# Kernel tuning notes

Hardware: AMD Instinct MI355X
Metric: run time of the kernel (lower is better)

The kernel has to match this reference:

```python
import jax, jax.numpy as jnp
import numpy as np

TEMPERATURE = 0.2
EPS = 1e-12

def _l2norm(x):
    # F.normalize(dim=1): x / max(||x||, eps)
    n = jnp.sqrt(jnp.sum(x * x, axis=1, keepdims=True))
    return x / jnp.maximum(n, EPS)

def setup_inputs() -> dict:
    key = jax.random.key(0)
    k1, k2, k3 = jax.random.split(key, 3)
    B, D, Q = 1024, 128, 65536
    return {
        "global_features_1": jax.random.normal(k1, (B, D), dtype=jnp.float32),
        "global_features_2": jax.random.normal(k2, (B, D), dtype=jnp.float32),
        "queue": jax.random.normal(k3, (Q, D), dtype=jnp.float32),
    }

def reference(global_features_1, global_features_2, queue):
    q = _l2norm(global_features_1)                    # [B, D]
    k = _l2norm(global_features_2)                    # [B, D]
    pos_sim = jnp.sum(q * k, axis=1, keepdims=True) / TEMPERATURE   # [B, 1]
    # queue renormalized under no_grad in the original
    queue_n = jax.lax.stop_gradient(_l2norm(queue))   # [Q, D]
    neg_sim = jnp.einsum('bd,qd->bq', q, queue_n) / TEMPERATURE     # [B, Q]
    logits = jnp.concatenate([pos_sim, neg_sim], axis=1)            # [B, 1+Q]
    # cross-entropy with label 0 for every row: -log_softmax(logits)[:, 0]
    log_probs = jax.nn.log_softmax(logits, axis=1)
    loss = -jnp.mean(log_probs[:, 0])
    return (loss, pos_sim, neg_sim)
```

## Files before the change

### kernel.cpp

```cpp
#include <hip/hip_runtime.h>
#include <math.h>

constexpr int B = 1024;
constexpr int D = 128;
constexpr int Q = 65536;
constexpr int NPART = 1024;
#define TEMP_INV 5.0f
#define EPS 1e-12f

typedef __bf16 bf16x8 __attribute__((ext_vector_type(8)));
typedef float  f32x4  __attribute__((ext_vector_type(4)));

__device__ __forceinline__ float wave_reduce_sum(float v) {
    #pragma unroll
    for (int off = 32; off > 0; off >>= 1) v += __shfl_xor(v, off);
    return v;
}

__device__ __forceinline__ unsigned short f2bf(float x) {
    unsigned int u = __float_as_uint(x);
    unsigned int r = (u + 0x7FFFu + ((u >> 16) & 1u)) >> 16;
    return (unsigned short)r;
}

__global__ __launch_bounds__(256) void k_prep(const float* __restrict__ g1,
                                              const float* __restrict__ g2,
                                              const float* __restrict__ queue,
                                              unsigned short* __restrict__ qnb,
                                              unsigned short* __restrict__ qb,
                                              float* __restrict__ out_pos,
                                              float* __restrict__ ws_pos) {
    if (blockIdx.x < Q / 8) {
        int half = threadIdx.x >> 5;
        int l    = threadIdx.x & 31;
        int row  = blockIdx.x * 8 + half;
        const f32x4* src = (const f32x4*)(queue + (size_t)row * D);
        f32x4 v = __builtin_nontemporal_load(&src[l]);
        float ss = v.x * v.x + v.y * v.y + v.z * v.z + v.w * v.w;
        #pragma unroll
        for (int off = 16; off > 0; off >>= 1) ss += __shfl_xor(ss, off);
        float inv = 1.0f / fmaxf(sqrtf(ss), EPS);
        uint2 o;
        o.x = (unsigned int)f2bf(v.x * inv) | ((unsigned int)f2bf(v.y * inv) << 16);
        o.y = (unsigned int)f2bf(v.z * inv) | ((unsigned int)f2bf(v.w * inv) << 16);
        ((uint2*)(qb + (size_t)row * D))[l] = o;
    } else {
        int idx = blockIdx.x - Q / 8;
        int w2 = threadIdx.x >> 7;
        int tt = threadIdx.x & 127;
        int b  = idx * 2 + w2;
        int w  = tt >> 6, lane = tt & 63;
        float x = g1[b * D + tt];
        float y = g2[b * D + tt];
        __shared__ float sx[2][2], sy[2][2], sp[2][2];
        float xs = wave_reduce_sum(x * x);
        float ys = wave_reduce_sum(y * y);
        if (lane == 0) { sx[w2][w] = xs; sy[w2][w] = ys; }
        __syncthreads();
        float ix = 1.0f / fmaxf(sqrtf(sx[w2][0] + sx[w2][1]), EPS);
        float iy = 1.0f / fmaxf(sqrtf(sy[w2][0] + sy[w2][1]), EPS);
        float qv = x * ix;
        float kv = y * iy;
        qnb[b * D + tt] = f2bf(qv);
        float p = wave_reduce_sum(qv * kv);
        if (lane == 0) sp[w2][w] = p;
        __syncthreads();
        if (tt == 0) {
            float pos = (sp[w2][0] + sp[w2][1]) * TEMP_INV;
            out_pos[b] = pos;
            ws_pos[b]  = pos;
        }
    }
}

__global__ __launch_bounds__(256, 3) void k_gemm_mfma(const unsigned short* __restrict__ qnb,
                                                      const unsigned short* __restrict__ qb,
                                                      float* __restrict__ neg,
                                                      float* __restrict__ psum) {
    __shared__ unsigned short As[128][72];
    __shared__ unsigned short Bs[128][72];
    const int t  = threadIdx.x;
    const int blk = blockIdx.x;
    const int bx = blk >> 3;
    const int by = blk & 7;
    const int R0 = by * 128, C0 = bx * 128;
    const int wid = t >> 6, lane = t & 63;
    const int wr = wid >> 1, wc = wid & 1;
    const int lg = lane >> 4, lc = lane & 15;

    f32x4 acc[4][4];
    #pragma unroll
    for (int m = 0; m < 4; ++m)
        #pragma unroll
        for (int n = 0; n < 4; ++n)
            #pragma unroll
            for (int r = 0; r < 4; ++r) acc[m][n][r] = 0.0f;

    #pragma unroll
    for (int s = 0; s < 2; ++s) {
        if (s) __syncthreads();
        const int ks = s * 64;
        #pragma unroll
        for (int p = 0; p < 4; ++p) {
            int c   = t + 256 * p;
            int row = c >> 3;
            int off = (c & 7) * 8;
            uint4 va = *(const uint4*)(qnb + (size_t)(R0 + row) * D + ks + off);
            uint4 vb = *(const uint4*)(qb  + (size_t)(C0 + row) * D + ks + off);
            *(uint4*)&As[row][off] = va;
            *(uint4*)&Bs[row][off] = vb;
        }
        __syncthreads();
        #pragma unroll
        for (int kk = 0; kk < 64; kk += 32) {
            int ko = kk + lg * 8;
            bf16x8 a[4], b[4];
            #pragma unroll
            for (int m = 0; m < 4; ++m)
                a[m] = *(const bf16x8*)&As[wr * 64 + m * 16 + lc][ko];
            #pragma unroll
            for (int n = 0; n < 4; ++n)
                b[n] = *(const bf16x8*)&Bs[wc * 64 + n * 16 + lc][ko];
            #pragma unroll
            for (int m = 0; m < 4; ++m)
                #pragma unroll
                for (int n = 0; n < 4; ++n)
                    acc[m][n] = __builtin_amdgcn_mfma_f32_16x16x32_bf16(a[m], b[n], acc[m][n], 0, 0, 0);
        }
    }

    float* Cs = (float*)&Bs[0][0];
    const int slot = bx * 2 + wc;
    #pragma unroll
    for (int m = 0; m < 4; ++m) {
        __syncthreads();
        #pragma unroll
        for (int reg = 0; reg < 4; ++reg) {
            float v0 = acc[m][0][reg] * TEMP_INV;
            float v1 = acc[m][1][reg] * TEMP_INV;
            float v2 = acc[m][2][reg] * TEMP_INV;
            float v3 = acc[m][3][reg] * TEMP_INV;
            int cr = (wr * 16 + lg * 4 + reg) * 132 + wc * 64 + lc;
            Cs[cr +  0] = v0;
            Cs[cr + 16] = v1;
            Cs[cr + 32] = v2;
            Cs[cr + 48] = v3;
            float e = __expf(v0 - 5.0f) + __expf(v1 - 5.0f) +
                      __expf(v2 - 5.0f) + __expf(v3 - 5.0f);
            #pragma unroll
            for (int off = 1; off < 16; off <<= 1) e += __shfl_xor(e, off);
            if (lc == 0) {
                int gr = R0 + wr * 64 + m * 16 + lg * 4 + reg;
                psum[(size_t)gr * NPART + slot] = e;
            }
        }
        __syncthreads();
        #pragma unroll
        for (int p = 0; p < 4; ++p) {
            int f  = t + 256 * p;
            int lr = f >> 5, c4 = f & 31;
            int gr = R0 + (lr >> 4) * 64 + m * 16 + (lr & 15);
            float4 o = *(const float4*)&Cs[lr * 132 + c4 * 4];
            *(float4*)(neg + (size_t)gr * Q + C0 + c4 * 4) = o;
        }
    }
}

__global__ __launch_bounds__(256) void k_reduce_lse(const float* __restrict__ psum,
                                                    const float* __restrict__ ws_pos,
                                                    float* __restrict__ loss_b) {
    int r = blockIdx.x;
    const float4* pr = (const float4*)(psum + (size_t)r * NPART);
    float4 v = pr[threadIdx.x];
    float s = v.x + v.y + v.z + v.w;
    s = wave_reduce_sum(s);
    __shared__ float sw[4];
    int w = threadIdx.x >> 6, lane = threadIdx.x & 63;
    if (lane == 0) sw[w] = s;
    __syncthreads();
    if (threadIdx.x == 0) {
        float S = sw[0] + sw[1] + sw[2] + sw[3];
        float pos = ws_pos[r];
        S += __expf(pos - 5.0f);
        loss_b[r] = (logf(S) + 5.0f) - pos;
    }
}

__global__ void k_loss_mean(const float* __restrict__ loss_b, float* __restrict__ out) {
    float s = 0.0f;
    for (int i = threadIdx.x; i < B; i += 256) s += loss_b[i];
    s = wave_reduce_sum(s);
    __shared__ float sw[4];
    int w = threadIdx.x >> 6, lane = threadIdx.x & 63;
    if (lane == 0) sw[w] = s;
    __syncthreads();
    if (threadIdx.x == 0) out[0] = (sw[0] + sw[1] + sw[2] + sw[3]) / (float)B;
}

extern "C" void kernel_launch(void* const* d_in, const int* in_sizes, int n_in,
                              void* d_out, int out_size, void* d_ws, size_t ws_size,
                              hipStream_t stream) {
    const float* g1    = (const float*)d_in[0];
    const float* g2    = (const float*)d_in[1];
    const float* queue = (const float*)d_in[2];
    float* out = (float*)d_out;

    float* out_pos = out + 1;
    float* neg     = out + 1 + B;

    unsigned short* qnb = (unsigned short*)d_ws;
    unsigned short* qb  = qnb + (size_t)B * D;
    float* psum   = (float*)(qb + (size_t)Q * D);
    float* ws_pos = psum + (size_t)B * NPART;
    float* loss_b = ws_pos + B;

    k_prep<<<Q / 8 + B / 2, 256, 0, stream>>>(g1, g2, queue, qnb, qb, out_pos, ws_pos);
    k_gemm_mfma<<<(Q / 128) * (B / 128), 256, 0, stream>>>(qnb, qb, neg, psum);
    k_reduce_lse<<<B, 256, 0, stream>>>(psum, ws_pos, loss_b);
    k_loss_mean<<<1, 256, 0, stream>>>(loss_b, out);
}
```

Baseline: 92.36 us.

## Fuse queue normalization and bf16 conversion into GEMM tile loads

The prep kernel now computes only per-row inverse norms of the queue and no longer writes a bf16 copy of the normalized queue. The GEMM reads the fp32 queue directly, scales it by the stored inverse norm and converts to bf16 while filling shared memory. This removes the 16 MB bf16 write and its reread. In exchange the GEMM loads twice as many bytes per B tile, and each queue tile is re-read by the 8 row-blocks that share a column. The nontemporal load in prep is dropped, presumably so the queue stays in cache for the GEMM.

```diff
diff --git a/kernel.cpp b/kernel.cpp
--- a/kernel.cpp
+++ b/kernel.cpp
@@ -27,7 +27,7 @@
                                               const float* __restrict__ g2,
                                               const float* __restrict__ queue,
                                               unsigned short* __restrict__ qnb,
-                                              unsigned short* __restrict__ qb,
+                                              float* __restrict__ qinv,
                                               float* __restrict__ out_pos,
                                               float* __restrict__ ws_pos) {
     if (blockIdx.x < Q / 8) {
@@ -35,15 +35,11 @@
         int l    = threadIdx.x & 31;
         int row  = blockIdx.x * 8 + half;
         const f32x4* src = (const f32x4*)(queue + (size_t)row * D);
-        f32x4 v = __builtin_nontemporal_load(&src[l]);
+        f32x4 v = src[l];
         float ss = v.x * v.x + v.y * v.y + v.z * v.z + v.w * v.w;
         #pragma unroll
         for (int off = 16; off > 0; off >>= 1) ss += __shfl_xor(ss, off);
-        float inv = 1.0f / fmaxf(sqrtf(ss), EPS);
-        uint2 o;
-        o.x = (unsigned int)f2bf(v.x * inv) | ((unsigned int)f2bf(v.y * inv) << 16);
-        o.y = (unsigned int)f2bf(v.z * inv) | ((unsigned int)f2bf(v.w * inv) << 16);
-        ((uint2*)(qb + (size_t)row * D))[l] = o;
+        if (l == 0) qinv[row] = 1.0f / fmaxf(sqrtf(ss), EPS);
     } else {
         int idx = blockIdx.x - Q / 8;
         int w2 = threadIdx.x >> 7;
@@ -74,7 +70,8 @@
 }
 
 __global__ __launch_bounds__(256, 3) void k_gemm_mfma(const unsigned short* __restrict__ qnb,
-                                                      const unsigned short* __restrict__ qb,
+                                                      const float* __restrict__ queue,
+                                                      const float* __restrict__ qinv,
                                                       float* __restrict__ neg,
                                                       float* __restrict__ psum) {
     __shared__ unsigned short As[128][72];
@@ -106,8 +103,16 @@
             int row = c >> 3;
             int off = (c & 7) * 8;
             uint4 va = *(const uint4*)(qnb + (size_t)(R0 + row) * D + ks + off);
-            uint4 vb = *(const uint4*)(qb  + (size_t)(C0 + row) * D + ks + off);
             *(uint4*)&As[row][off] = va;
+            const float* qrow = queue + (size_t)(C0 + row) * D + ks + off;
+            float inv = qinv[C0 + row];
+            f32x4 u0 = *(const f32x4*)(qrow);
+            f32x4 u1 = *(const f32x4*)(qrow + 4);
+            uint4 vb;
+            vb.x = (unsigned int)f2bf(u0.x * inv) | ((unsigned int)f2bf(u0.y * inv) << 16);
+            vb.y = (unsigned int)f2bf(u0.z * inv) | ((unsigned int)f2bf(u0.w * inv) << 16);
+            vb.z = (unsigned int)f2bf(u1.x * inv) | ((unsigned int)f2bf(u1.y * inv) << 16);
+            vb.w = (unsigned int)f2bf(u1.z * inv) | ((unsigned int)f2bf(u1.w * inv) << 16);
             *(uint4*)&Bs[row][off] = vb;
         }
         __syncthreads();
@@ -209,13 +214,13 @@
     float* neg     = out + 1 + B;
 
     unsigned short* qnb = (unsigned short*)d_ws;
-    unsigned short* qb  = qnb + (size_t)B * D;
-    float* psum   = (float*)(qb + (size_t)Q * D);
+    float* qinv   = (float*)(qnb + (size_t)B * D);
+    float* psum   = qinv + Q;
     float* ws_pos = psum + (size_t)B * NPART;
     float* loss_b = ws_pos + B;
 
-    k_prep<<<Q / 8 + B / 2, 256, 0, stream>>>(g1, g2, queue, qnb, qb, out_pos, ws_pos);
-    k_gemm_mfma<<<(Q / 128) * (B / 128), 256, 0, stream>>>(qnb, qb, neg, psum);
+    k_prep<<<Q / 8 + B / 2, 256, 0, stream>>>(g1, g2, queue, qnb, qinv, out_pos, ws_pos);
+    k_gemm_mfma<<<(Q / 128) * (B / 128), 256, 0, stream>>>(qnb, queue, qinv, neg, psum);
     k_reduce_lse<<<B, 256, 0, stream>>>(psum, ws_pos, loss_b);
     k_loss_mean<<<1, 256, 0, stream>>>(loss_b, out);
 }
```

After: 107.8 us. 16.7% more time.
